# Kernel optimization log

Hardware: AMD Instinct MI355X
Metric: run time of the kernel (lower is better)

The kernel has to match this reference:

```python
import jax, jax.numpy as jnp
import numpy as np

D = 1024      # input_size
H = 16        # num_heads
HD = D // H   # head_dim
B, S = 8, 1024


def setup_inputs() -> dict:
    key = jax.random.key(0)
    ks = jax.random.split(key, 9)
    s = 1.0 / np.sqrt(D)
    return {
        "x": jax.random.normal(ks[0], (B, S, D), dtype=jnp.float32),
        "Wq": jax.random.uniform(ks[1], (D, D), jnp.float32, -s, s),
        "bq": jax.random.uniform(ks[2], (D,), jnp.float32, -s, s),
        "Wk": jax.random.uniform(ks[3], (D, D), jnp.float32, -s, s),
        "bk": jax.random.uniform(ks[4], (D,), jnp.float32, -s, s),
        "Wv": jax.random.uniform(ks[5], (D, D), jnp.float32, -s, s),
        "bv": jax.random.uniform(ks[6], (D,), jnp.float32, -s, s),
        "Wf": jax.random.uniform(ks[7], (D, D), jnp.float32, -s, s),
        "bf": jax.random.uniform(ks[8], (D,), jnp.float32, -s, s),
    }


def reference(x, Wq, bq, Wk, bk, Wv, bv, Wf, bf):
    b, s, d = x.shape
    # torch Linear: x @ W.T + b; split into heads -> [b, H, s, HD]
    def split(y):
        return y.reshape(b, s, H, HD).transpose(0, 2, 1, 3)
    q = split(x @ Wq.T + bq)
    k = split(x @ Wk.T + bk)
    v = split(x @ Wv.T + bv)
    scores = jnp.einsum("bhqd,bhkd->bhqk", q, k) / jnp.sqrt(jnp.float32(HD))
    probs = jax.nn.softmax(scores, axis=-1)
    ctx = jnp.einsum("bhqk,bhkd->bhqd", probs, v)
    ctx = ctx.transpose(0, 2, 1, 3).reshape(b, s, d)
    out = ctx @ Wf.T + bf
    return (out, probs)
```

## Files before the change

### kernel.cpp

```cpp
#include <hip/hip_runtime.h>

typedef __bf16 bf16;
typedef __bf16 bf16x4 __attribute__((ext_vector_type(4)));
typedef __bf16 bf16x8 __attribute__((ext_vector_type(8)));
typedef float  f32x4  __attribute__((ext_vector_type(4)));

constexpr int Bb = 8, Ss = 1024, Dd = 1024, Hh = 16, HDd = 64;
constexpr int Mm = Bb * Ss;
constexpr int Kk = 1024;

struct CastArgs {
  const float* src[5];
  bf16* dst[5];
  int cum[5];
};
__global__ void cast_all(CastArgs a, int tot) {
  int i = blockIdx.x * blockDim.x + threadIdx.x;
  if (i >= tot) return;
  int s, base;
  if (i < a.cum[0])      { s = 0; base = 0; }
  else if (i < a.cum[1]) { s = 1; base = a.cum[0]; }
  else if (i < a.cum[2]) { s = 2; base = a.cum[1]; }
  else if (i < a.cum[3]) { s = 3; base = a.cum[2]; }
  else                   { s = 4; base = a.cum[3]; }
  int j = i - base;
  float4 v = reinterpret_cast<const float4*>(a.src[s])[j];
  bf16x4 o = { (bf16)v.x, (bf16)v.y, (bf16)v.z, (bf16)v.w };
  reinterpret_cast<bf16x4*>(a.dst[s])[j] = o;
}

__device__ __forceinline__ void gemm_loop(const bf16* __restrict__ A, const bf16* __restrict__ Bm,
                                          int bm, int bn, unsigned char* As, unsigned char* Bs,
                                          int w, int lane, int l15, int g, f32x4 (&acc)[4][4]) {
  const bf16* srcA[4];
  const bf16* srcB[4];
#pragma unroll
  for (int i = 0; i < 4; ++i) {
    int gch = (w * 4 + i) * 64 + lane;
    int r = gch >> 3, c = gch & 7, cs = c ^ (r & 7);
    srcA[i] = A  + (size_t)(bm * 128 + r) * Kk + cs * 8;
    srcB[i] = Bm + (size_t)(bn * 128 + r) * Kk + cs * 8;
  }
  for (int kt = 0; kt < Kk / 64; ++kt) {
    __syncthreads();
#pragma unroll
    for (int i = 0; i < 4; ++i) {
      __builtin_amdgcn_global_load_lds(
          (const __attribute__((address_space(1))) void*)(srcA[i] + kt * 64),
          (__attribute__((address_space(3))) void*)(As + (w * 4 + i) * 1024), 16, 0, 0);
      __builtin_amdgcn_global_load_lds(
          (const __attribute__((address_space(1))) void*)(srcB[i] + kt * 64),
          (__attribute__((address_space(3))) void*)(Bs + (w * 4 + i) * 1024), 16, 0, 0);
    }
    __syncthreads();
#pragma unroll
    for (int kk = 0; kk < 2; ++kk) {
      const int kb = kk * 64 + g * 16;
      bf16x8 af[4], bfr[4];
#pragma unroll
      for (int mi = 0; mi < 4; ++mi) {
        int row = ((w >> 1) * 64) + mi * 16 + l15;
        af[mi] = *reinterpret_cast<const bf16x8*>(As + row * 128 + (kb ^ ((row & 7) << 4)));
      }
#pragma unroll
      for (int ni = 0; ni < 4; ++ni) {
        int row = ((w & 1) * 64) + ni * 16 + l15;
        bfr[ni] = *reinterpret_cast<const bf16x8*>(Bs + row * 128 + (kb ^ ((row & 7) << 4)));
      }
#pragma unroll
      for (int mi = 0; mi < 4; ++mi)
#pragma unroll
        for (int ni = 0; ni < 4; ++ni)
          acc[mi][ni] = __builtin_amdgcn_mfma_f32_16x16x32_bf16(af[mi], bfr[ni], acc[mi][ni], 0, 0, 0);
    }
  }
}

__global__ __launch_bounds__(256) void gemm_qkv(const bf16* __restrict__ x,
                                                const bf16* __restrict__ wq, const bf16* __restrict__ wk,
                                                const bf16* __restrict__ wv,
                                                const float* __restrict__ bq, const float* __restrict__ bk,
                                                const float* __restrict__ bv,
                                                bf16* __restrict__ Qo, bf16* __restrict__ Ko,
                                                bf16* __restrict__ Vto) {
  const int tid = threadIdx.x;
  const int lane = tid & 63;
  const int w = tid >> 6;
  const int l15 = lane & 15, g = lane >> 4;
  const int z = blockIdx.z;

  const bf16* A; const bf16* Bm; int bm, bn;
  if (z < 2) { A = x; Bm = z ? wk : wq; bm = blockIdx.x; bn = blockIdx.y; }
  else       { A = wv; Bm = x;          bm = blockIdx.y; bn = blockIdx.x; }

  __shared__ __align__(16) unsigned char As[128 * 128];
  __shared__ __align__(16) unsigned char Bs[128 * 128];
  f32x4 acc[4][4] = {};
  gemm_loop(A, Bm, bm, bn, As, Bs, w, lane, l15, g, acc);

  const int wr = (w >> 1) * 64, wc = (w & 1) * 64;
  if (z < 2) {
    const float* bias = z ? bk : bq;
    bf16* out = z ? Ko : Qo;
    const float scale = z ? 1.f : 0.125f;
#pragma unroll
    for (int ni = 0; ni < 4; ++ni) {
      int col = bn * 128 + wc + ni * 16 + l15;
      float bv_ = bias[col];
#pragma unroll
      for (int mi = 0; mi < 4; ++mi)
#pragma unroll
        for (int r = 0; r < 4; ++r) {
          int row = bm * 128 + wr + mi * 16 + g * 4 + r;
          float val = (acc[mi][ni][r] + bv_) * scale;
          size_t adr = ((size_t)((row >> 10) * Hh + (col >> 6)) * Ss + (row & 1023)) * HDd + (col & 63);
          out[adr] = (bf16)val;
        }
    }
  } else {
#pragma unroll
    for (int mi = 0; mi < 4; ++mi)
#pragma unroll
      for (int r = 0; r < 4; ++r) {
        int row = bm * 128 + wr + mi * 16 + g * 4 + r;
        float bv_ = bv[row];
#pragma unroll
        for (int ni = 0; ni < 4; ++ni) {
          int col = bn * 128 + wc + ni * 16 + l15;
          size_t adr = ((size_t)((col >> 10) * Hh + (row >> 6)) * HDd + (row & 63)) * Ss + (col & 1023);
          Vto[adr] = (bf16)(acc[mi][ni][r] + bv_);
        }
      }
  }
}

__global__ __launch_bounds__(256) void gemm_out(const bf16* __restrict__ A, const bf16* __restrict__ Bm,
                                                const float* __restrict__ bias, float* __restrict__ out) {
  const int tid = threadIdx.x;
  const int lane = tid & 63;
  const int w = tid >> 6;
  const int l15 = lane & 15, g = lane >> 4;
  const int bn = blockIdx.x, bm = blockIdx.y;
  __shared__ __align__(16) unsigned char As[128 * 128];
  __shared__ __align__(16) unsigned char Bs[128 * 128];
  f32x4 acc[4][4] = {};
  gemm_loop(A, Bm, bm, bn, As, Bs, w, lane, l15, g, acc);
  const int wr = (w >> 1) * 64, wc = (w & 1) * 64;
#pragma unroll
  for (int ni = 0; ni < 4; ++ni) {
    int col = bn * 128 + wc + ni * 16 + l15;
    float bv_ = bias[col];
#pragma unroll
    for (int mi = 0; mi < 4; ++mi)
#pragma unroll
      for (int r = 0; r < 4; ++r) {
        int row = bm * 128 + wr + mi * 16 + g * 4 + r;
        out[(size_t)row * Dd + col] = acc[mi][ni][r] + bv_;
      }
  }
}

#define WAITV(n) asm volatile("s_waitcnt vmcnt(" #n ")" ::: "memory")
#define PHASE_BAR { __builtin_amdgcn_s_barrier(); __builtin_amdgcn_sched_barrier(0); }

__global__ __launch_bounds__(512, 4) void attn_fused(const bf16* __restrict__ Q,
                                                     const bf16* __restrict__ Kt,
                                                     const bf16* __restrict__ Vt,
                                                     float* __restrict__ probs,
                                                     bf16* __restrict__ ctx) {
  const int tid = threadIdx.x;
  const int lane = tid & 63;
  const int w = tid >> 6;
  const int l15 = lane & 15, g = lane >> 4;
  const int bid = blockIdx.x;
  const int bh = (bid & 7) * 16 + ((bid >> 3) & 15);
  const int qt = bid >> 7;
  const int q0 = qt * 128 + w * 16;

  __shared__ __align__(16) unsigned char KV[4][16384];
  __shared__ __align__(16) bf16 Ps[8][16][40];

  bf16x8 qf0, qf1;
  {
    const bf16* qp = Q + ((size_t)bh * Ss + q0 + l15) * HDd + g * 8;
    qf0 = *reinterpret_cast<const bf16x8*>(qp);
    qf1 = *reinterpret_cast<const bf16x8*>(qp + 32);
  }
  const bf16* kbase = Kt + (size_t)bh * Ss * HDd;
  const bf16* vbase = Vt + (size_t)bh * HDd * Ss;

  const bf16* ksrc[2];
  const bf16* vsrc[2];
#pragma unroll
  for (int i = 0; i < 2; ++i) {
    int ch = i * 512 + tid;
    int kr = ch >> 3, kc = (ch & 7) ^ (kr & 7);
    ksrc[i] = kbase + (size_t)kr * HDd + kc * 8;
    int vr = ch >> 4, vc = (ch & 15) ^ (vr & 15);
    vsrc[i] = vbase + (size_t)vr * Ss + vc * 8;
  }

#define SK(slab, t)                                                                       \
  {                                                                                       \
    _Pragma("unroll") for (int i = 0; i < 2; ++i)                                         \
        __builtin_amdgcn_global_load_lds(                                                 \
            (const __attribute__((address_space(1))) void*)(ksrc[i] + (size_t)(t) * 128 * HDd), \
            (__attribute__((address_space(3))) void*)(KV[slab] + (i * 512 + w * 64) * 16),\
            16, 0, 0);                                                                    \
  }
#define SV(slab, t)                                                                       \
  {                                                                                       \
    _Pragma("unroll") for (int i = 0; i < 2; ++i)                                         \
        __builtin_amdgcn_global_load_lds(                                                 \
            (const __attribute__((address_space(1))) void*)(vsrc[i] + (t) * 128),         \
            (__attribute__((address_space(3))) void*)(KV[slab] + (i * 512 + w * 64) * 16),\
            16, 0, 0);                                                                    \
  }

  auto kread = [&](int slab, int nk, int half) -> bf16x8 {
    int row = nk * 16 + l15;
    int chunk = (half * 4 + g) ^ (l15 & 7);
    return *reinterpret_cast<const bf16x8*>(KV[slab] + row * 128 + chunk * 16);
  };
  auto vread = [&](int slab, int nkp, int ni) -> bf16x8 {
    int row = ni * 16 + l15;
    int chunk = (nkp * 4 + g) ^ l15;
    return *reinterpret_cast<const bf16x8*>(KV[slab] + row * 256 + chunk * 16);
  };

  float lr0 = 0.f, lr1 = 0.f, lr2 = 0.f, lr3 = 0.f;
  SK(0, 0); SK(1, 1); SK(2, 2);
  __builtin_amdgcn_sched_barrier(0);
  WAITV(4);
  PHASE_BAR;
  for (int kt = 0; kt < 8; ++kt) {
    if (kt <= 4)      { SK((kt + 3) & 3, kt + 3); }
    else if (kt == 7) { SK(0, 0); SV(2, 0); }
    __builtin_amdgcn_sched_barrier(0);
    const int ks = kt & 3;
#pragma unroll
    for (int nk = 0; nk < 8; ++nk) {
      f32x4 sc = {0.f, 0.f, 0.f, 0.f};
      bf16x8 k0 = kread(ks, nk, 0), k1 = kread(ks, nk, 1);
      __builtin_amdgcn_s_setprio(1);
      sc = __builtin_amdgcn_mfma_f32_16x16x32_bf16(k0, qf0, sc, 0, 0, 0);
      sc = __builtin_amdgcn_mfma_f32_16x16x32_bf16(k1, qf1, sc, 0, 0, 0);
      __builtin_amdgcn_s_setprio(0);
      lr0 += __expf(sc[0]); lr1 += __expf(sc[1]);
      lr2 += __expf(sc[2]); lr3 += __expf(sc[3]);
    }
    if (kt <= 4)      { WAITV(4); }
    else if (kt == 5) { WAITV(2); }
    else              { WAITV(0); }
    PHASE_BAR;
  }
  float lsum = (lr0 + lr1) + (lr2 + lr3);
  lsum += __shfl_xor(lsum, 16, 64);
  lsum += __shfl_xor(lsum, 32, 64);
  const float rl = 1.f / lsum;

  float* const prow = probs + ((size_t)bh * Ss + q0 + l15) * Ss;
  f32x4 cacc[4] = {};

  for (int kt = 0; kt < 8; ++kt) {
    if (kt < 7) { SK((kt + 1) & 1, kt + 1); SV(2 + ((kt + 1) & 1), kt + 1); }
    __builtin_amdgcn_sched_barrier(0);
    const int ks = kt & 1, vs = 2 + (kt & 1);
#pragma unroll
    for (int nkp = 0; nkp < 4; ++nkp) {
#pragma unroll
      for (int h = 0; h < 2; ++h) {
        int nk = nkp * 2 + h;
        f32x4 sc = {0.f, 0.f, 0.f, 0.f};
        bf16x8 k0 = kread(ks, nk, 0), k1 = kread(ks, nk, 1);
        __builtin_amdgcn_s_setprio(1);
        sc = __builtin_amdgcn_mfma_f32_16x16x32_bf16(k0, qf0, sc, 0, 0, 0);
        sc = __builtin_amdgcn_mfma_f32_16x16x32_bf16(k1, qf1, sc, 0, 0, 0);
        __builtin_amdgcn_s_setprio(0);
        f32x4 pv;
#pragma unroll
        for (int r = 0; r < 4; ++r) pv[r] = __expf(sc[r]) * rl;
        *reinterpret_cast<f32x4*>(prow + kt * 128 + nk * 16 + g * 4) = pv;
        bf16x4 pb = { (bf16)pv[0], (bf16)pv[1], (bf16)pv[2], (bf16)pv[3] };
        *reinterpret_cast<bf16x4*>(&Ps[w][l15][h * 16 + g * 4]) = pb;
      }
      bf16x8 pf = *reinterpret_cast<const bf16x8*>(&Ps[w][l15][g * 8]);
      bf16x8 vf0 = vread(vs, nkp, 0), vf1 = vread(vs, nkp, 1);
      bf16x8 vf2 = vread(vs, nkp, 2), vf3 = vread(vs, nkp, 3);
      __builtin_amdgcn_s_setprio(1);
      cacc[0] = __builtin_amdgcn_mfma_f32_16x16x32_bf16(pf, vf0, cacc[0], 0, 0, 0);
      cacc[1] = __builtin_amdgcn_mfma_f32_16x16x32_bf16(pf, vf1, cacc[1], 0, 0, 0);
      cacc[2] = __builtin_amdgcn_mfma_f32_16x16x32_bf16(pf, vf2, cacc[2], 0, 0, 0);
      cacc[3] = __builtin_amdgcn_mfma_f32_16x16x32_bf16(pf, vf3, cacc[3], 0, 0, 0);
      __builtin_amdgcn_s_setprio(0);
    }
    if (kt < 7) {
      WAITV(8);
      PHASE_BAR;
    }
  }
#undef SK
#undef SV

  const int bb = bh >> 4, hh = bh & 15;
#pragma unroll
  for (int ni = 0; ni < 4; ++ni)
#pragma unroll
    for (int r = 0; r < 4; ++r) {
      int q = q0 + g * 4 + r;
      ctx[((size_t)bb * Ss + q) * Dd + hh * 64 + ni * 16 + l15] = (bf16)cacc[ni][r];
    }
}

extern "C" void kernel_launch(void* const* d_in, const int* in_sizes, int n_in,
                              void* d_out, int out_size, void* d_ws, size_t ws_size,
                              hipStream_t stream) {
  (void)in_sizes; (void)n_in; (void)out_size; (void)ws_size;
  const float* x   = (const float*)d_in[0];
  const float* Wq  = (const float*)d_in[1];
  const float* bq  = (const float*)d_in[2];
  const float* Wk  = (const float*)d_in[3];
  const float* bk  = (const float*)d_in[4];
  const float* Wv  = (const float*)d_in[5];
  const float* bv  = (const float*)d_in[6];
  const float* Wf  = (const float*)d_in[7];
  const float* bfp = (const float*)d_in[8];

  char* ws = (char*)d_ws;
  size_t off = 0;
  auto alloc = [&](size_t n) { void* p = ws + off; off += (n + 255) & ~(size_t)255; return p; };
  bf16* xb   = (bf16*)alloc((size_t)Mm * Dd * 2);
  bf16* wqb  = (bf16*)alloc((size_t)Dd * Dd * 2);
  bf16* wkb  = (bf16*)alloc((size_t)Dd * Dd * 2);
  bf16* wvb  = (bf16*)alloc((size_t)Dd * Dd * 2);
  bf16* wfb  = (bf16*)alloc((size_t)Dd * Dd * 2);
  bf16* Qb   = (bf16*)alloc((size_t)Mm * Dd * 2);
  bf16* Kb   = (bf16*)alloc((size_t)Mm * Dd * 2);
  bf16* Vtb  = (bf16*)alloc((size_t)Mm * Dd * 2);
  bf16* ctxb = (bf16*)alloc((size_t)Mm * Dd * 2);

  CastArgs ca;
  ca.src[0] = x;  ca.dst[0] = xb;  int n0 = Mm * Dd / 4;
  ca.src[1] = Wq; ca.dst[1] = wqb; int nw = Dd * Dd / 4;
  ca.src[2] = Wk; ca.dst[2] = wkb;
  ca.src[3] = Wv; ca.dst[3] = wvb;
  ca.src[4] = Wf; ca.dst[4] = wfb;
  ca.cum[0] = n0; ca.cum[1] = n0 + nw; ca.cum[2] = n0 + 2 * nw;
  ca.cum[3] = n0 + 3 * nw; ca.cum[4] = n0 + 4 * nw;
  int tot = ca.cum[4];
  cast_all<<<(tot + 255) / 256, 256, 0, stream>>>(ca, tot);

  gemm_qkv<<<dim3(Mm / 128, Dd / 128, 3), 256, 0, stream>>>(xb, wqb, wkb, wvb, bq, bk, bv, Qb, Kb, Vtb);

  float* probs = (float*)d_out + (size_t)Mm * Dd;
  attn_fused<<<dim3(Bb * Hh * 8), 512, 0, stream>>>(Qb, Kb, Vtb, probs, ctxb);

  gemm_out<<<dim3(Dd / 128, Mm / 128), 256, 0, stream>>>(ctxb, wfb, bfp, (float*)d_out);
}
```

Before: 263.8 us.

## Read K directly from global in softmax-sum pass and fold log2e into Q scale

The first attention pass, which accumulates row sums of exp(scores), now loads K fragments straight from global memory into registers instead of staging them through an LDS ring with async loads and barriers. The first K/V slabs for the second pass are prefetched into LDS while this pass runs, and a __syncthreads separates the two passes. The Q projection scale now includes log2(e), so both passes can use the hardware exp2 instruction instead of __expf. This removes the LDS traffic and per-tile barriers from the first pass. In exchange it depends on L1/L2 absorbing the repeated global K reads, and the register loads are neither swizzled nor scheduled.

```diff
diff --git a/kernel.cpp b/kernel.cpp
--- a/kernel.cpp
+++ b/kernel.cpp
@@ -102,7 +102,7 @@
   if (z < 2) {
     const float* bias = z ? bk : bq;
     bf16* out = z ? Ko : Qo;
-    const float scale = z ? 1.f : 0.125f;
+    const float scale = z ? 1.f : 0.125f * 1.44269504088896340736f;
 #pragma unroll
     for (int ni = 0; ni < 4; ++ni) {
       int col = bn * 128 + wc + ni * 16 + l15;
@@ -229,35 +229,32 @@
   };
 
   float lr0 = 0.f, lr1 = 0.f, lr2 = 0.f, lr3 = 0.f;
-  SK(0, 0); SK(1, 1); SK(2, 2);
-  __builtin_amdgcn_sched_barrier(0);
-  WAITV(4);
-  PHASE_BAR;
-  for (int kt = 0; kt < 8; ++kt) {
-    if (kt <= 4)      { SK((kt + 3) & 3, kt + 3); }
-    else if (kt == 7) { SK(0, 0); SV(2, 0); }
-    __builtin_amdgcn_sched_barrier(0);
-    const int ks = kt & 3;
-#pragma unroll
-    for (int nk = 0; nk < 8; ++nk) {
-      f32x4 sc = {0.f, 0.f, 0.f, 0.f};
-      bf16x8 k0 = kread(ks, nk, 0), k1 = kread(ks, nk, 1);
-      __builtin_amdgcn_s_setprio(1);
-      sc = __builtin_amdgcn_mfma_f32_16x16x32_bf16(k0, qf0, sc, 0, 0, 0);
-      sc = __builtin_amdgcn_mfma_f32_16x16x32_bf16(k1, qf1, sc, 0, 0, 0);
-      __builtin_amdgcn_s_setprio(0);
-      lr0 += __expf(sc[0]); lr1 += __expf(sc[1]);
-      lr2 += __expf(sc[2]); lr3 += __expf(sc[3]);
-    }
-    if (kt <= 4)      { WAITV(4); }
-    else if (kt == 5) { WAITV(2); }
-    else              { WAITV(0); }
-    PHASE_BAR;
+  SK(0, 0); SV(2, 0);
+  {
+    const bf16* const kf = kbase + (size_t)l15 * HDd + g * 8;
+    for (int kt = 0; kt < 8; ++kt) {
+#pragma unroll
+      for (int nk = 0; nk < 8; ++nk) {
+        const bf16* kp = kf + (size_t)(kt * 128 + nk * 16) * HDd;
+        bf16x8 k0 = *reinterpret_cast<const bf16x8*>(kp);
+        bf16x8 k1 = *reinterpret_cast<const bf16x8*>(kp + 32);
+        f32x4 sc = {0.f, 0.f, 0.f, 0.f};
+        sc = __builtin_amdgcn_mfma_f32_16x16x32_bf16(k0, qf0, sc, 0, 0, 0);
+        sc = __builtin_amdgcn_mfma_f32_16x16x32_bf16(k1, qf1, sc, 0, 0, 0);
+        lr0 += __builtin_amdgcn_exp2f(sc[0]);
+        lr1 += __builtin_amdgcn_exp2f(sc[1]);
+        lr2 += __builtin_amdgcn_exp2f(sc[2]);
+        lr3 += __builtin_amdgcn_exp2f(sc[3]);
+      }
+    }
   }
   float lsum = (lr0 + lr1) + (lr2 + lr3);
   lsum += __shfl_xor(lsum, 16, 64);
   lsum += __shfl_xor(lsum, 32, 64);
   const float rl = 1.f / lsum;
+
+  __syncthreads();
+  __builtin_amdgcn_sched_barrier(0);
 
   float* const prow = probs + ((size_t)bh * Ss + q0 + l15) * Ss;
   f32x4 cacc[4] = {};
@@ -279,7 +276,7 @@
         __builtin_amdgcn_s_setprio(0);
         f32x4 pv;
 #pragma unroll
-        for (int r = 0; r < 4; ++r) pv[r] = __expf(sc[r]) * rl;
+        for (int r = 0; r < 4; ++r) pv[r] = __builtin_amdgcn_exp2f(sc[r]) * rl;
         *reinterpret_cast<f32x4*>(prow + kt * 128 + nk * 16 + g * 4) = pv;
         bf16x4 pb = { (bf16)pv[0], (bf16)pv[1], (bf16)pv[2], (bf16)pv[3] };
         *reinterpret_cast<bf16x4*>(&Ps[w][l15][h * 16 + g * 4]) = pb;
```

After: 325.8 us. 23.5% more time.

## Swizzle GEMM block IDs per XCD and fold log2e into Q scale for exp2

Applied to the files above, without the earlier changes.

Both GEMM launches now use a flat 1D grid whose block index is remapped so each of the 8 XCDs works on a contiguous group of row tiles. Blocks that share A rows therefore share that XCD's L2. The Q projection scale now includes log2(e), so the attention softmax can use the hardware exp2 instruction instead of __expf and skip the extra multiply. The remapping hardcodes the tile counts and the 8-XCD round-robin dispatch assumption.

```diff
diff --git a/kernel.cpp b/kernel.cpp
--- a/kernel.cpp
+++ b/kernel.cpp
@@ -87,11 +87,17 @@
   const int lane = tid & 63;
   const int w = tid >> 6;
   const int l15 = lane & 15, g = lane >> 4;
-  const int z = blockIdx.z;
+
+  const int id = blockIdx.x;
+  const int xcd = id & 7, slot = id >> 3;
+  const int bmg = slot / 24, rem = slot % 24;
+  const int bmx = xcd * 8 + bmg;
+  const int bnx = rem & 7;
+  const int z = rem >> 3;
 
   const bf16* A; const bf16* Bm; int bm, bn;
-  if (z < 2) { A = x; Bm = z ? wk : wq; bm = blockIdx.x; bn = blockIdx.y; }
-  else       { A = wv; Bm = x;          bm = blockIdx.y; bn = blockIdx.x; }
+  if (z < 2) { A = x; Bm = z ? wk : wq; bm = bmx; bn = bnx; }
+  else       { A = wv; Bm = x;          bm = bnx; bn = bmx; }
 
   __shared__ __align__(16) unsigned char As[128 * 128];
   __shared__ __align__(16) unsigned char Bs[128 * 128];
@@ -102,7 +108,7 @@
   if (z < 2) {
     const float* bias = z ? bk : bq;
     bf16* out = z ? Ko : Qo;
-    const float scale = z ? 1.f : 0.125f;
+    const float scale = z ? 1.f : 0.125f * 1.44269504088896340736f;
 #pragma unroll
     for (int ni = 0; ni < 4; ++ni) {
       int col = bn * 128 + wc + ni * 16 + l15;
@@ -140,7 +146,10 @@
   const int lane = tid & 63;
   const int w = tid >> 6;
   const int l15 = lane & 15, g = lane >> 4;
-  const int bn = blockIdx.x, bm = blockIdx.y;
+  const int id = blockIdx.x;
+  const int xcd = id & 7, slot = id >> 3;
+  const int bm = xcd * 8 + (slot >> 3);
+  const int bn = slot & 7;
   __shared__ __align__(16) unsigned char As[128 * 128];
   __shared__ __align__(16) unsigned char Bs[128 * 128];
   f32x4 acc[4][4] = {};
@@ -246,8 +255,10 @@
       sc = __builtin_amdgcn_mfma_f32_16x16x32_bf16(k0, qf0, sc, 0, 0, 0);
       sc = __builtin_amdgcn_mfma_f32_16x16x32_bf16(k1, qf1, sc, 0, 0, 0);
       __builtin_amdgcn_s_setprio(0);
-      lr0 += __expf(sc[0]); lr1 += __expf(sc[1]);
-      lr2 += __expf(sc[2]); lr3 += __expf(sc[3]);
+      lr0 += __builtin_amdgcn_exp2f(sc[0]);
+      lr1 += __builtin_amdgcn_exp2f(sc[1]);
+      lr2 += __builtin_amdgcn_exp2f(sc[2]);
+      lr3 += __builtin_amdgcn_exp2f(sc[3]);
     }
     if (kt <= 4)      { WAITV(4); }
     else if (kt == 5) { WAITV(2); }
@@ -279,7 +290,7 @@
         __builtin_amdgcn_s_setprio(0);
         f32x4 pv;
 #pragma unroll
-        for (int r = 0; r < 4; ++r) pv[r] = __expf(sc[r]) * rl;
+        for (int r = 0; r < 4; ++r) pv[r] = __builtin_amdgcn_exp2f(sc[r]) * rl;
         *reinterpret_cast<f32x4*>(prow + kt * 128 + nk * 16 + g * 4) = pv;
         bf16x4 pb = { (bf16)pv[0], (bf16)pv[1], (bf16)pv[2], (bf16)pv[3] };
         *reinterpret_cast<bf16x4*>(&Ps[w][l15][h * 16 + g * 4]) = pb;
@@ -350,10 +361,10 @@
   int tot = ca.cum[4];
   cast_all<<<(tot + 255) / 256, 256, 0, stream>>>(ca, tot);
 
-  gemm_qkv<<<dim3(Mm / 128, Dd / 128, 3), 256, 0, stream>>>(xb, wqb, wkb, wvb, bq, bk, bv, Qb, Kb, Vtb);
+  gemm_qkv<<<dim3(64 * 8 * 3), 256, 0, stream>>>(xb, wqb, wkb, wvb, bq, bk, bv, Qb, Kb, Vtb);
 
   float* probs = (float*)d_out + (size_t)Mm * Dd;
   attn_fused<<<dim3(Bb * Hh * 8), 512, 0, stream>>>(Qb, Kb, Vtb, probs, ctxb);
 
-  gemm_out<<<dim3(Dd / 128, Mm / 128), 256, 0, stream>>>(ctxb, wfb, bfp, (float*)d_out);
-}
+  gemm_out<<<dim3(64 * 8), 256, 0, stream>>>(ctxb, wfb, bfp, (float*)d_out);
+}
```

Result: no change. 261.5 us (-0.9%).
